# Kernel optimization log

Measured on AMD Instinct MI355X. Metric: run time of the kernel, lower is better.

The kernel has to match this reference:

```python
import jax, jax.numpy as jnp
import numpy as np

B, H, W, C = 16, 64, 64, 256
WIN, SHIFT, HEADS, NSTYLE, HID = 8, 4, 8, 512, 1024
HB = HEADS // 2   # heads per attention branch
CB = C // 2       # channels per branch
N = WIN * WIN     # tokens per window
EPS = 1e-5


def _rel_index(w):
    coords = np.stack(np.meshgrid(np.arange(w), np.arange(w), indexing='ij'))  # [2,w,w]
    cf = coords.reshape(2, -1)
    rel = (cf[:, :, None] - cf[:, None, :]).transpose(1, 2, 0)  # [N,N,2]
    rel[:, :, 0] += w - 1
    rel[:, :, 1] += w - 1
    rel[:, :, 0] *= 2 * w - 1
    return rel.sum(-1)  # [N,N]


def _sw_mask(Hh, Ww, w, shift):
    img = np.zeros((Hh, Ww))
    cnt = 0
    for hs in (slice(0, -w), slice(-w, -shift), slice(-shift, None)):
        for ws in (slice(0, -w), slice(-w, -shift), slice(-shift, None)):
            img[hs, ws] = cnt
            cnt += 1
    win = img.reshape(Hh // w, w, Ww // w, w).transpose(0, 2, 1, 3).reshape(-1, w * w)
    m = win[:, None, :] - win[:, :, None]
    return np.where(m != 0, -100.0, 0.0).astype(np.float32)  # [nW,N,N]


REL_IDX = _rel_index(WIN)
SW_MASK = jnp.asarray(_sw_mask(H, W, WIN, SHIFT))


def window_partition(x):
    # x: [B,H,W,c] -> [B*nW, N, c]
    b, hh, ww, c = x.shape
    x = x.reshape(b, hh // WIN, WIN, ww // WIN, WIN, c).transpose(0, 1, 3, 2, 4, 5)
    return x.reshape(-1, N, c)


def window_reverse(win):
    c = win.shape[-1]
    x = win.reshape(B, H // WIN, W // WIN, WIN, WIN, c).transpose(0, 1, 3, 2, 4, 5)
    return x.reshape(B, H, W, c)


def _adain(x, style, Wa, ba):
    # x: [B,L,C]; instance norm over L per channel, then style affine
    s = style @ Wa + ba                      # [B, 2C]
    mu_s, std_s = jnp.split(s, 2, axis=1)    # each [B,C]
    mu = x.mean(axis=1, keepdims=True)
    var = ((x - mu) ** 2).mean(axis=1, keepdims=True)
    xn = (x - mu) * jax.lax.rsqrt(var + EPS)
    return mu_s[:, None, :] + std_s[:, None, :] * xn


def _win_attn(q, k, v, rpb, mask):
    # q,k,v: [B_, N, CB]; rpb: [(2w-1)^2, HB]; mask: [nW,N,N] or None
    B_ = q.shape[0]
    d = CB // HB
    q = q.reshape(B_, N, HB, d).transpose(0, 2, 1, 3) * (d ** -0.5)
    k = k.reshape(B_, N, HB, d).transpose(0, 2, 1, 3)
    v = v.reshape(B_, N, HB, d).transpose(0, 2, 1, 3)
    attn = jnp.einsum('bhnd,bhmd->bhnm', q, k)
    bias = rpb[REL_IDX.reshape(-1)].reshape(N, N, HB).transpose(2, 0, 1)
    attn = attn + bias[None]
    if mask is not None:
        nW = mask.shape[0]
        attn = attn.reshape(B_ // nW, nW, HB, N, N) + mask[None, :, None]
        attn = attn.reshape(B_, HB, N, N)
    attn = jax.nn.softmax(attn, axis=-1)
    out = jnp.einsum('bhnm,bhmd->bhnd', attn, v)
    return out.transpose(0, 2, 1, 3).reshape(B_, N, CB)


def setup_inputs() -> dict:
    key = jax.random.key(0)
    ks = jax.random.split(key, 20)
    f = jnp.float32
    return {
        'x': jax.random.normal(ks[0], (B, H * W, C), f),
        'style': jax.random.normal(ks[1], (B, NSTYLE), f),
        'w_qkv': jax.random.normal(ks[2], (C, 3 * C), f) * 0.02,
        'b_qkv': jnp.zeros((3 * C,), f),
        'w_proj': jax.random.normal(ks[3], (C, C), f) * 0.02,
        'b_proj': jnp.zeros((C,), f),
        'w_ada1': jax.random.normal(ks[4], (NSTYLE, 2 * C), f) * 0.02,
        'b_ada1': jnp.concatenate([jnp.zeros((C,), f), jnp.ones((C,), f)]),
        'w_ada2': jax.random.normal(ks[5], (NSTYLE, 2 * C), f) * 0.02,
        'b_ada2': jnp.concatenate([jnp.zeros((C,), f), jnp.ones((C,), f)]),
        'rpb1': jax.random.normal(ks[6], ((2 * WIN - 1) ** 2, HB), f) * 0.02,
        'rpb2': jax.random.normal(ks[7], ((2 * WIN - 1) ** 2, HB), f) * 0.02,
        'w_fc1': jax.random.normal(ks[8], (C, HID), f) * 0.02,
        'b_fc1': jnp.zeros((HID,), f),
        'w_fc2': jax.random.normal(ks[9], (HID, C), f) * 0.02,
        'b_fc2': jnp.zeros((C,), f),
    }


def reference(x, style, w_qkv, b_qkv, w_proj, b_proj, w_ada1, b_ada1,
              w_ada2, b_ada2, rpb1, rpb2, w_fc1, b_fc1, w_fc2, b_fc2):
    Bn, L, Cc = x.shape
    # AdaIN 1
    h = _adain(x, style, w_ada1, b_ada1)                      # [B,L,C]
    qkv = (h @ w_qkv + b_qkv).reshape(Bn, H, W, 3, Cc)
    q, k, v = qkv[..., 0, :], qkv[..., 1, :], qkv[..., 2, :]  # [B,H,W,C]
    # split channels across the two branches
    q1, k1, v1 = q[..., :CB], k[..., :CB], v[..., :CB]
    q2, k2, v2 = q[..., CB:], k[..., CB:], v[..., CB:]
    shift = lambda t: jnp.roll(t, (-SHIFT, -SHIFT), axis=(1, 2))
    # W-MSA branch
    x_w = _win_attn(window_partition(q1), window_partition(k1),
                    window_partition(v1), rpb1, None)
    # SW-MSA branch (shifted windows + mask)
    x_sw = _win_attn(window_partition(shift(q2)), window_partition(shift(k2)),
                     window_partition(shift(v2)), rpb2, SW_MASK)
    xw = window_reverse(x_w)                                  # [B,H,W,CB]
    xsw = jnp.roll(window_reverse(x_sw), (SHIFT, SHIFT), axis=(1, 2))
    attn_out = jnp.concatenate([xw, xsw], axis=-1).reshape(Bn, L, Cc)
    x = x + attn_out @ w_proj + b_proj
    # AdaIN 2 + MLP (exact GELU, as nn.GELU default)
    h2 = _adain(x, style, w_ada2, b_ada2)
    h2 = jax.nn.gelu(h2 @ w_fc1 + b_fc1, approximate=False)
    return x + (h2 @ w_fc2 + b_fc2)
```

## Files before the change

### kernel.cpp

```cpp
#include <hip/hip_runtime.h>
#include <hip/hip_bf16.h>

typedef __bf16 bf16;
typedef __bf16 bf16x4v __attribute__((ext_vector_type(4)));
typedef __bf16 bf16x8v __attribute__((ext_vector_type(8)));
typedef float f32x4 __attribute__((ext_vector_type(4)));
typedef short s16x4 __attribute__((ext_vector_type(4)));

#define DEVINL static __device__ __forceinline__

DEVINL f32x4 mfma16(bf16x8v a, bf16x8v b, f32x4 c) {
  return __builtin_amdgcn_mfma_f32_16x16x32_bf16(a, b, c, 0, 0, 0);
}

DEVINL f32x4 mfma16x16(bf16x4v a, bf16x4v b, f32x4 c) {
#if __has_builtin(__builtin_amdgcn_mfma_f32_16x16x16bf16_1k)
  return __builtin_amdgcn_mfma_f32_16x16x16bf16_1k(
      __builtin_bit_cast(s16x4, a), __builtin_bit_cast(s16x4, b), c, 0, 0, 0);
#else
  f32x4 d;
  asm("v_mfma_f32_16x16x16_bf16 %0, %1, %2, %3"
      : "=v"(d) : "v"(a), "v"(b), "v"(c));
  return d;
#endif
}

__global__ __launch_bounds__(256) void k_style(
    const float* __restrict__ style,
    const float* __restrict__ wa1, const float* __restrict__ ba1,
    const float* __restrict__ wa2, const float* __restrict__ ba2,
    float* __restrict__ s1, float* __restrict__ s2) {
  int bid = blockIdx.x;
  int ng = bid & 31, b = (bid >> 5) & 15, which = bid >> 9;
  int tid = threadIdx.x;
  int nl = tid & 15, kg = tid >> 4;
  int n = ng * 16 + nl;
  const float* wa = which ? wa2 : wa1;
  const float* ba = which ? ba2 : ba1;
  const float* srow = style + b * 512;
  float acc = 0.f;
  #pragma unroll 8
  for (int kk = 0; kk < 32; ++kk) {
    int k = kg + kk * 16;
    acc += srow[k] * wa[k * 512 + n];
  }
  acc += __shfl_xor(acc, 16);
  acc += __shfl_xor(acc, 32);
  __shared__ float red[4][16];
  int l = tid & 63, w = tid >> 6;
  if (l < 16) red[w][nl] = acc;
  __syncthreads();
  if (tid < 16) {
    float S = red[0][tid] + red[1][tid] + red[2][tid] + red[3][tid]
            + ba[ng * 16 + tid];
    (which ? s2 : s1)[b * 512 + ng * 16 + tid] = S;
  }
}

template<int F32>
__global__ __launch_bounds__(256) void k_stats_part(
    const void* __restrict__ xv, float* __restrict__ psum,
    float* __restrict__ psq) {
  int rc = blockIdx.x, b = blockIdx.y;
  int c = threadIdx.x;
  size_t base = (size_t)b * 4096 * 256 + (size_t)rc * 256 * 256 + c;
  float sm = 0.f, q = 0.f;
  #pragma unroll 4
  for (int r = 0; r < 256; ++r) {
    float f;
    if constexpr (F32) f = ((const float*)xv)[base + (size_t)r * 256];
    else               f = (float)((const bf16*)xv)[base + (size_t)r * 256];
    sm += f; q += f * f;
  }
  int o = (b * 16 + rc) * 256 + c;
  psum[o] = sm; psq[o] = q;
}

__global__ __launch_bounds__(256) void k_stats_fin(
    const float* __restrict__ psum, const float* __restrict__ psq,
    const float* __restrict__ s,
    float* __restrict__ scale, float* __restrict__ shift) {
  int b = blockIdx.x, c = threadIdx.x;
  float S = 0.f, Q = 0.f;
  #pragma unroll
  for (int rc = 0; rc < 16; ++rc) {
    S += psum[(b * 16 + rc) * 256 + c];
    Q += psq[(b * 16 + rc) * 256 + c];
  }
  float mean = S * (1.0f/4096.0f);
  float var  = Q * (1.0f/4096.0f) - mean * mean;
  float inv  = rsqrtf(var + 1e-5f);
  float mu_s  = s[b * 512 + c];
  float std_s = s[b * 512 + 256 + c];
  float sc = std_s * inv;
  scale[b * 256 + c] = sc;
  shift[b * 256 + c] = mu_s - sc * mean;
}

template<int F32>
__global__ __launch_bounds__(256) void k_adain(
    const void* __restrict__ in, const float* __restrict__ scale,
    const float* __restrict__ shift, bf16* __restrict__ out) {
  int idx = blockIdx.x * 256 + threadIdx.x;
  int c8 = idx & 31, row = idx >> 5;
  int b = row >> 12, c = c8 * 8;
  const float* scp = &scale[b * 256 + c];
  const float* shp = &shift[b * 256 + c];
  f32x4 sc0 = *(const f32x4*)scp, sc1 = *(const f32x4*)(scp + 4);
  f32x4 sh0 = *(const f32x4*)shp, sh1 = *(const f32x4*)(shp + 4);
  size_t ofs = (size_t)row * 256 + c;
  float f[8];
  if constexpr (F32) {
    f32x4 v0 = *(const f32x4*)&((const float*)in)[ofs];
    f32x4 v1 = *(const f32x4*)&((const float*)in)[ofs + 4];
    f[0]=v0[0]; f[1]=v0[1]; f[2]=v0[2]; f[3]=v0[3];
    f[4]=v1[0]; f[5]=v1[1]; f[6]=v1[2]; f[7]=v1[3];
  } else {
    bf16x8v v = *(const bf16x8v*)&((const bf16*)in)[ofs];
    #pragma unroll
    for (int u = 0; u < 8; ++u) f[u] = (float)v[u];
  }
  bf16x8v o;
  o[0]=(bf16)(sh0[0]+sc0[0]*f[0]); o[1]=(bf16)(sh0[1]+sc0[1]*f[1]);
  o[2]=(bf16)(sh0[2]+sc0[2]*f[2]); o[3]=(bf16)(sh0[3]+sc0[3]*f[3]);
  o[4]=(bf16)(sh1[0]+sc1[0]*f[4]); o[5]=(bf16)(sh1[1]+sc1[1]*f[5]);
  o[6]=(bf16)(sh1[2]+sc1[2]*f[6]); o[7]=(bf16)(sh1[3]+sc1[3]*f[7]);
  *(bf16x8v*)&out[ofs] = o;
}

__global__ __launch_bounds__(256) void k_tr(
    const float* __restrict__ in, bf16* __restrict__ out, int K, int N) {
  __shared__ float t[32][33];
  int bx = blockIdx.x * 32, by = blockIdx.y * 32;
  int tx = threadIdx.x & 31, ty = threadIdx.x >> 5;
  #pragma unroll
  for (int r = 0; r < 32; r += 8)
    t[ty + r][tx] = in[(size_t)(by + ty + r) * N + bx + tx];
  __syncthreads();
  #pragma unroll
  for (int r = 0; r < 32; r += 8)
    out[(size_t)(bx + ty + r) * K + by + tx] = (bf16)t[tx][ty + r];
}

DEVINL void stage_lds(bf16* dst, const bf16* __restrict__ src, int ld,
                      int row0, int k0, int tid) {
  int w = tid >> 6, l = tid & 63;
  #pragma unroll
  for (int i = 0; i < 4; ++i) {
    int slot = i * 256 + w * 64 + l;
    int r = slot >> 3, cs = slot & 7;
    int c = cs ^ (r & 7);
    const bf16* g = src + (size_t)(row0 + r) * ld + k0 + c * 8;
    __builtin_amdgcn_global_load_lds(
        (const __attribute__((address_space(1))) void*)g,
        (__attribute__((address_space(3))) void*)(dst + (i * 256 + w * 64) * 8),
        16, 0, 0);
  }
}

template<int RESMODE, int GELU, int OUTF32>
__global__ __launch_bounds__(256) void k_gemm(
    const bf16* __restrict__ A, const bf16* __restrict__ Bt,
    const float* __restrict__ bias, const void* __restrict__ resv,
    void* __restrict__ outv, int N, int K, int gx) {
  __shared__ bf16 a_sw[128 * 64];
  __shared__ bf16 b_sw[128 * 64];
  int tid = threadIdx.x;
  int l = tid & 63, w = tid >> 6;
  int wr = w >> 1, wc = w & 1;
  int lm = l & 15, lg = l >> 4;

  int nwg = gridDim.x;
  int lin = blockIdx.x;
  int swz = (lin & 7) * (nwg >> 3) + (lin >> 3);
  int bx = swz % gx, by = swz / gx;
  int m0 = by * 128, n0 = bx * 128;

  f32x4 acc[4][4];
  #pragma unroll
  for (int mi = 0; mi < 4; ++mi)
    #pragma unroll
    for (int ni = 0; ni < 4; ++ni)
      acc[mi][ni] = (f32x4){0.f, 0.f, 0.f, 0.f};

  for (int k0 = 0; k0 < K; k0 += 64) {
    stage_lds(a_sw, A, K, m0, k0, tid);
    stage_lds(b_sw, Bt, K, n0, k0, tid);
    __syncthreads();
    #pragma unroll
    for (int kk = 0; kk < 2; ++kk) {
      bf16x8v af[4], bv[4];
      #pragma unroll
      for (int mi = 0; mi < 4; ++mi) {
        int row = wr * 64 + mi * 16 + lm;
        af[mi] = *(const bf16x8v*)&a_sw[row * 64 + (((kk * 4 + lg) ^ (row & 7)) * 8)];
      }
      #pragma unroll
      for (int ni = 0; ni < 4; ++ni) {
        int row = wc * 64 + ni * 16 + lm;
        bv[ni] = *(const bf16x8v*)&b_sw[row * 64 + (((kk * 4 + lg) ^ (row & 7)) * 8)];
      }
      #pragma unroll
      for (int mi = 0; mi < 4; ++mi)
        #pragma unroll
        for (int ni = 0; ni < 4; ++ni)
          acc[mi][ni] = mfma16(af[mi], bv[ni], acc[mi][ni]);
    }
    __syncthreads();
  }
  #pragma unroll
  for (int mi = 0; mi < 4; ++mi) {
    #pragma unroll
    for (int ni = 0; ni < 4; ++ni) {
      int row = m0 + wr * 64 + mi * 16 + lg * 4;
      int col = n0 + wc * 64 + ni * 16 + lm;
      float bv_ = bias[col];
      #pragma unroll
      for (int j = 0; j < 4; ++j) {
        float o = acc[mi][ni][j] + bv_;
        if constexpr (RESMODE == 1)
          o += ((const float*)resv)[(size_t)(row + j) * N + col];
        if constexpr (RESMODE == 2)
          o += (float)((const bf16*)resv)[(size_t)(row + j) * N + col];
        if constexpr (GELU) {
          float z = 1.5957691216057308f * (o + 0.044715f * o * o * o);
          o = o / (1.0f + __expf(-z));
        }
        if constexpr (OUTF32)
          ((float*)outv)[(size_t)(row + j) * N + col] = o;
        else
          ((bf16*)outv)[(size_t)(row + j) * N + col] = (bf16)o;
      }
    }
  }
}

__global__ __launch_bounds__(256) void k_attn(
    const bf16* __restrict__ qkv,
    const float* __restrict__ rpb1, const float* __restrict__ rpb2,
    bf16* __restrict__ aout) {
  __shared__ bf16 vt[128 * 72];
  __shared__ float rl[960];

  int tid = threadIdx.x;
  int bx = blockIdx.x;
  int br = bx & 1, widx = (bx >> 1) & 63, b = bx >> 7;
  int wy = widx >> 3, wx = widx & 7;

  const float* rpb = br ? rpb2 : rpb1;
  #pragma unroll
  for (int t = tid; t < 960; t += 256) {
    int h0 = t / 240, r0 = t - h0 * 240, dy = r0 >> 4, dx = r0 & 15;
    rl[t] = (dx < 15) ? rpb[(dy * 15 + dx) * 4 + h0] : 0.f;
  }

  auto grow = [&](int tok) -> int {
    int y = wy * 8 + (tok >> 3), xc = wx * 8 + (tok & 7);
    if (br) { y = (y + 4) & 63; xc = (xc + 4) & 63; }
    return b * 4096 + y * 64 + xc;
  };

  #pragma unroll
  for (int it = 0; it < 4; ++it) {
    int task = it * 256 + tid;
    int tok = task & 63, chunk = task >> 6;
    bf16x8v v = *(const bf16x8v*)&qkv[(size_t)grow(tok) * 768 + 512 + br * 128 + chunk * 8];
    #pragma unroll
    for (int u = 0; u < 8; ++u) vt[(chunk * 8 + u) * 72 + tok] = v[u];
  }

  int l = tid & 63, h = tid >> 6;
  int lm = l & 15, lg = l >> 4;

  bf16x8v kb[4], qa[4];
  #pragma unroll
  for (int i = 0; i < 4; ++i) {
    size_t rb = (size_t)grow(i * 16 + lm) * 768 + br * 128 + h * 32 + lg * 8;
    qa[i] = *(const bf16x8v*)&qkv[rb];
    kb[i] = *(const bf16x8v*)&qkv[rb + 256];
  }
  __syncthreads();

  bf16x4v vb[2][4];
  #pragma unroll
  for (int ni = 0; ni < 2; ++ni)
    #pragma unroll
    for (int ki = 0; ki < 4; ++ki)
      vb[ni][ki] = *(const bf16x4v*)&vt[(h * 32 + ni * 16 + lm) * 72 + ki * 16 + lg * 4];

  bool need_mask = br && (wy == 7 || wx == 7);

  int ekA[16], idkA[16];
  #pragma unroll
  for (int ki = 0; ki < 4; ++ki)
    #pragma unroll
    for (int j = 0; j < 4; ++j) {
      int ik = ki * 16 + lg * 4 + j;
      ekA[ki * 4 + j] = ik + (ik >> 3) * 8;
      int yk = wy * 8 + (ik >> 3), xk = wx * 8 + (ik & 7);
      idkA[ki * 4 + j] = (yk < 56 ? 0 : (yk < 60 ? 1 : 2)) * 3
                       + (xk < 56 ? 0 : (xk < 60 ? 1 : 2));
    }

  #pragma unroll
  for (int qi = 0; qi < 4; ++qi) {
    f32x4 s[4];
    #pragma unroll
    for (int ki = 0; ki < 4; ++ki)
      s[ki] = mfma16(kb[ki], qa[qi], (f32x4){0.f,0.f,0.f,0.f});

    int iq = qi * 16 + lm;
    int eq = iq + (iq >> 3) * 8;
    int yq = wy * 8 + (iq >> 3), xq = wx * 8 + (iq & 7);
    int idq = (yq < 56 ? 0 : (yq < 60 ? 1 : 2)) * 3
            + (xq < 56 ? 0 : (xq < 60 ? 1 : 2));
    const float* fb = &rl[h * 240 + 119 + eq];

    #pragma unroll
    for (int ki = 0; ki < 4; ++ki)
      #pragma unroll
      for (int j = 0; j < 4; ++j) {
        float val = s[ki][j] * 0.17677669529663687f + fb[-ekA[ki * 4 + j]];
        if (need_mask && idq != idkA[ki * 4 + j]) val -= 100.0f;
        s[ki][j] = val;
      }

    float mx = s[0][0];
    #pragma unroll
    for (int ki = 0; ki < 4; ++ki)
      #pragma unroll
      for (int j = 0; j < 4; ++j) mx = fmaxf(mx, s[ki][j]);
    mx = fmaxf(mx, __shfl_xor(mx, 16));
    mx = fmaxf(mx, __shfl_xor(mx, 32));
    float sum = 0.f;
    #pragma unroll
    for (int ki = 0; ki < 4; ++ki)
      #pragma unroll
      for (int j = 0; j < 4; ++j) {
        float e = __expf(s[ki][j] - mx);
        s[ki][j] = e;
        sum += e;
      }
    sum += __shfl_xor(sum, 16);
    sum += __shfl_xor(sum, 32);
    float rs = 1.0f / sum;

    bf16x4v pa[4];
    #pragma unroll
    for (int ki = 0; ki < 4; ++ki)
      #pragma unroll
      for (int j = 0; j < 4; ++j)
        pa[ki][j] = (bf16)(s[ki][j] * rs);

    f32x4 o[2] = {(f32x4){0.f,0.f,0.f,0.f}, (f32x4){0.f,0.f,0.f,0.f}};
    #pragma unroll
    for (int ki = 0; ki < 4; ++ki) {
      o[0] = mfma16x16(pa[ki], vb[0][ki], o[0]);
      o[1] = mfma16x16(pa[ki], vb[1][ki], o[1]);
    }

    #pragma unroll
    for (int ni = 0; ni < 2; ++ni)
      #pragma unroll
      for (int j = 0; j < 4; ++j) {
        int tok = qi * 16 + lg * 4 + j;
        int col = br * 128 + h * 32 + ni * 16 + lm;
        aout[(size_t)grow(tok) * 256 + col] = (bf16)o[ni][j];
      }
  }
}

extern "C" void kernel_launch(void* const* d_in, const int* in_sizes, int n_in,
                              void* d_out, int out_size, void* d_ws, size_t ws_size,
                              hipStream_t stream) {
  (void)in_sizes; (void)n_in; (void)out_size; (void)ws_size;
  const float* x      = (const float*)d_in[0];
  const float* style  = (const float*)d_in[1];
  const float* w_qkv  = (const float*)d_in[2];
  const float* b_qkv  = (const float*)d_in[3];
  const float* w_proj = (const float*)d_in[4];
  const float* b_proj = (const float*)d_in[5];
  const float* w_ada1 = (const float*)d_in[6];
  const float* b_ada1 = (const float*)d_in[7];
  const float* w_ada2 = (const float*)d_in[8];
  const float* b_ada2 = (const float*)d_in[9];
  const float* rpb1   = (const float*)d_in[10];
  const float* rpb2   = (const float*)d_in[11];
  const float* w_fc1  = (const float*)d_in[12];
  const float* b_fc1  = (const float*)d_in[13];
  const float* w_fc2  = (const float*)d_in[14];
  const float* b_fc2  = (const float*)d_in[15];

  char* ws = (char*)d_ws;
  float* s1     = (float*)(ws + 0);
  float* s2     = (float*)(ws + 32768);
  float* scale1 = (float*)(ws + 65536);
  float* shift1 = (float*)(ws + 81920);
  float* scale2 = (float*)(ws + 98304);
  float* shift2 = (float*)(ws + 114688);
  bf16* wtqkv   = (bf16*)(ws + 131072);
  bf16* wtproj  = (bf16*)(ws + 524288);
  bf16* wtfc1   = (bf16*)(ws + 655360);
  bf16* wtfc2   = (bf16*)(ws + 1179648);
  float* psum   = (float*)(ws + 1703936);
  float* psq    = (float*)(ws + 1966080);
  const size_t BIG = 2228224;
  bf16* xn   = (bf16*)(ws + BIG);
  bf16* qkv  = (bf16*)(ws + BIG + 33554432);
  bf16* attn = (bf16*)(ws + BIG + 134217728);
  bf16* x1   = (bf16*)(ws + BIG + 33554432);
  bf16* xn2  = xn;
  bf16* g    = (bf16*)(ws + BIG + 67108864);

  k_tr<<<dim3(24, 8),  256, 0, stream>>>(w_qkv,  wtqkv,  256, 768);
  k_tr<<<dim3(8, 8),   256, 0, stream>>>(w_proj, wtproj, 256, 256);
  k_tr<<<dim3(32, 8),  256, 0, stream>>>(w_fc1,  wtfc1,  256, 1024);
  k_tr<<<dim3(8, 32),  256, 0, stream>>>(w_fc2,  wtfc2,  1024, 256);

  k_style<<<1024, 256, 0, stream>>>(style, w_ada1, b_ada1, w_ada2, b_ada2, s1, s2);
  k_stats_part<1><<<dim3(16, 16), 256, 0, stream>>>(x, psum, psq);
  k_stats_fin<<<16, 256, 0, stream>>>(psum, psq, s1, scale1, shift1);
  k_adain<1><<<8192, 256, 0, stream>>>(x, scale1, shift1, xn);

  k_gemm<0,0,0><<<3072, 256, 0, stream>>>(
      xn, wtqkv, b_qkv, nullptr, qkv, 768, 256, 6);

  k_attn<<<2048, 256, 0, stream>>>(qkv, rpb1, rpb2, attn);

  k_gemm<1,0,0><<<1024, 256, 0, stream>>>(
      attn, wtproj, b_proj, x, x1, 256, 256, 2);

  k_stats_part<0><<<dim3(16, 16), 256, 0, stream>>>(x1, psum, psq);
  k_stats_fin<<<16, 256, 0, stream>>>(psum, psq, s2, scale2, shift2);
  k_adain<0><<<8192, 256, 0, stream>>>(x1, scale2, shift2, xn2);

  for (int ch = 0; ch < 2; ++ch) {
    size_t ro = (size_t)ch * 32768;
    k_gemm<0,1,0><<<2048, 256, 0, stream>>>(
        xn2 + ro * 256, wtfc1, b_fc1, nullptr, g, 1024, 256, 8);
    k_gemm<2,0,1><<<512, 256, 0, stream>>>(
        g, wtfc2, b_fc2, x1 + ro * 256,
        (float*)d_out + ro * 256, 256, 1024, 2);
  }
}
```

Baseline: 339.6 us.

## Stream A operands from global and stage only B in LDS with 256x64 tiles

```diff
diff --git a/kernel.cpp b/kernel.cpp
--- a/kernel.cpp
+++ b/kernel.cpp
@@ -8,6 +8,8 @@
 typedef short s16x4 __attribute__((ext_vector_type(4)));
 
 #define DEVINL static __device__ __forceinline__
+#define AS1 __attribute__((address_space(1)))
+#define AS3 __attribute__((address_space(3)))
 
 DEVINL f32x4 mfma16(bf16x8v a, bf16x8v b, f32x4 c) {
   return __builtin_amdgcn_mfma_f32_16x16x32_bf16(a, b, c, 0, 0, 0);
@@ -142,39 +144,26 @@
     out[(size_t)(bx + ty + r) * K + by + tx] = (bf16)t[tx][ty + r];
 }
 
-DEVINL void stage_lds(bf16* dst, const bf16* __restrict__ src, int ld,
-                      int row0, int k0, int tid) {
-  int w = tid >> 6, l = tid & 63;
-  #pragma unroll
-  for (int i = 0; i < 4; ++i) {
-    int slot = i * 256 + w * 64 + l;
-    int r = slot >> 3, cs = slot & 7;
-    int c = cs ^ (r & 7);
-    const bf16* g = src + (size_t)(row0 + r) * ld + k0 + c * 8;
-    __builtin_amdgcn_global_load_lds(
-        (const __attribute__((address_space(1))) void*)g,
-        (__attribute__((address_space(3))) void*)(dst + (i * 256 + w * 64) * 8),
-        16, 0, 0);
-  }
-}
-
 template<int RESMODE, int GELU, int OUTF32>
-__global__ __launch_bounds__(256) void k_gemm(
+__global__ __launch_bounds__(256) void k_gemm_stream(
     const bf16* __restrict__ A, const bf16* __restrict__ Bt,
     const float* __restrict__ bias, const void* __restrict__ resv,
     void* __restrict__ outv, int N, int K, int gx) {
-  __shared__ bf16 a_sw[128 * 64];
-  __shared__ bf16 b_sw[128 * 64];
+  __shared__ bf16 b_sw[64 * 256];
   int tid = threadIdx.x;
   int l = tid & 63, w = tid >> 6;
-  int wr = w >> 1, wc = w & 1;
   int lm = l & 15, lg = l >> 4;
 
   int nwg = gridDim.x;
   int lin = blockIdx.x;
   int swz = (lin & 7) * (nwg >> 3) + (lin >> 3);
   int bx = swz % gx, by = swz / gx;
-  int m0 = by * 128, n0 = bx * 128;
+  int m0 = by * 256, n0 = bx * 64;
+
+  const bf16* pA[4];
+  #pragma unroll
+  for (int mi = 0; mi < 4; ++mi)
+    pA[mi] = A + (size_t)(m0 + w * 64 + mi * 16 + lm) * K + lg * 8;
 
   f32x4 acc[4][4];
   #pragma unroll
@@ -183,22 +172,30 @@
     for (int ni = 0; ni < 4; ++ni)
       acc[mi][ni] = (f32x4){0.f, 0.f, 0.f, 0.f};
 
-  for (int k0 = 0; k0 < K; k0 += 64) {
-    stage_lds(a_sw, A, K, m0, k0, tid);
-    stage_lds(b_sw, Bt, K, n0, k0, tid);
+  for (int ks = 0; ks < K; ks += 256) {
+    if (ks) __syncthreads();
+    #pragma unroll
+    for (int i = 0; i < 8; ++i) {
+      int slot = i * 256 + tid;
+      int r = slot >> 5, c = slot & 31;
+      int cs = c ^ (r & 7);
+      const bf16* g = Bt + (size_t)(n0 + r) * K + ks + cs * 8;
+      __builtin_amdgcn_global_load_lds(
+          (const AS1 void*)g,
+          (AS3 void*)(b_sw + (size_t)(i * 256 + w * 64) * 8), 16, 0, 0);
+    }
     __syncthreads();
-    #pragma unroll
-    for (int kk = 0; kk < 2; ++kk) {
+
+    #pragma unroll
+    for (int kk = 0; kk < 8; ++kk) {
       bf16x8v af[4], bv[4];
       #pragma unroll
-      for (int mi = 0; mi < 4; ++mi) {
-        int row = wr * 64 + mi * 16 + lm;
-        af[mi] = *(const bf16x8v*)&a_sw[row * 64 + (((kk * 4 + lg) ^ (row & 7)) * 8)];
-      }
+      for (int mi = 0; mi < 4; ++mi)
+        af[mi] = *(const bf16x8v*)(pA[mi] + ks + kk * 32);
       #pragma unroll
       for (int ni = 0; ni < 4; ++ni) {
-        int row = wc * 64 + ni * 16 + lm;
-        bv[ni] = *(const bf16x8v*)&b_sw[row * 64 + (((kk * 4 + lg) ^ (row & 7)) * 8)];
+        int row = ni * 16 + lm;
+        bv[ni] = *(const bf16x8v*)&b_sw[row * 256 + (((kk * 4 + lg) ^ (row & 7)) * 8)];
       }
       #pragma unroll
       for (int mi = 0; mi < 4; ++mi)
@@ -206,14 +203,14 @@
         for (int ni = 0; ni < 4; ++ni)
           acc[mi][ni] = mfma16(af[mi], bv[ni], acc[mi][ni]);
     }
-    __syncthreads();
-  }
+  }
+
   #pragma unroll
   for (int mi = 0; mi < 4; ++mi) {
     #pragma unroll
     for (int ni = 0; ni < 4; ++ni) {
-      int row = m0 + wr * 64 + mi * 16 + lg * 4;
-      int col = n0 + wc * 64 + ni * 16 + lm;
+      int row = m0 + w * 64 + mi * 16 + lg * 4;
+      int col = n0 + ni * 16 + lm;
       float bv_ = bias[col];
       #pragma unroll
       for (int j = 0; j < 4; ++j) {
@@ -422,13 +419,13 @@
   k_stats_fin<<<16, 256, 0, stream>>>(psum, psq, s1, scale1, shift1);
   k_adain<1><<<8192, 256, 0, stream>>>(x, scale1, shift1, xn);
 
-  k_gemm<0,0,0><<<3072, 256, 0, stream>>>(
-      xn, wtqkv, b_qkv, nullptr, qkv, 768, 256, 6);
+  k_gemm_stream<0,0,0><<<3072, 256, 0, stream>>>(
+      xn, wtqkv, b_qkv, nullptr, qkv, 768, 256, 12);
 
   k_attn<<<2048, 256, 0, stream>>>(qkv, rpb1, rpb2, attn);
 
-  k_gemm<1,0,0><<<1024, 256, 0, stream>>>(
-      attn, wtproj, b_proj, x, x1, 256, 256, 2);
+  k_gemm_stream<1,0,0><<<1024, 256, 0, stream>>>(
+      attn, wtproj, b_proj, x, x1, 256, 256, 4);
 
   k_stats_part<0><<<dim3(16, 16), 256, 0, stream>>>(x1, psum, psq);
   k_stats_fin<<<16, 256, 0, stream>>>(psum, psq, s2, scale2, shift2);
@@ -436,10 +433,10 @@
 
   for (int ch = 0; ch < 2; ++ch) {
     size_t ro = (size_t)ch * 32768;
-    k_gemm<0,1,0><<<2048, 256, 0, stream>>>(
-        xn2 + ro * 256, wtfc1, b_fc1, nullptr, g, 1024, 256, 8);
-    k_gemm<2,0,1><<<512, 256, 0, stream>>>(
+    k_gemm_stream<0,1,0><<<2048, 256, 0, stream>>>(
+        xn2 + ro * 256, wtfc1, b_fc1, nullptr, g, 1024, 256, 16);
+    k_gemm_stream<2,0,1><<<512, 256, 0, stream>>>(
         g, wtfc2, b_fc2, x1 + ro * 256,
-        (float*)d_out + ro * 256, 256, 1024, 2);
-  }
-}
+        (float*)d_out + ro * 256, 256, 1024, 4);
+  }
+}
```

New measurement: 436.0 us. +28.4%, slower.
